# Performance work log

Measured on AMD Instinct MI355X. Metric: run time of the kernel, lower is better.

The kernel has to match this reference:

```python
import jax, jax.numpy as jnp
import numpy as np

NUM_HEADS = 8
GROUPS = 8
EPS = 1e-5


def setup_inputs() -> dict:
    key = jax.random.key(0)
    ks = jax.random.split(key, 5)
    B, C, H, W = 2, 512, 64, 64
    x = jax.random.normal(ks[0], (B, C, H, W), dtype=jnp.float32)
    gn_w = jnp.ones((C,), dtype=jnp.float32)
    gn_b = jnp.zeros((C,), dtype=jnp.float32)
    qkv_w = jax.random.normal(ks[1], (3 * C, C), dtype=jnp.float32) * 0.02  # 1x1 conv weight
    qkv_b = jnp.zeros((3 * C,), dtype=jnp.float32)
    proj_w = jax.random.normal(ks[2], (C, C), dtype=jnp.float32) * 0.02
    proj_b = jnp.zeros((C,), dtype=jnp.float32)
    return {"x": x, "gn_w": gn_w, "gn_b": gn_b, "qkv_w": qkv_w,
            "qkv_b": qkv_b, "proj_w": proj_w, "proj_b": proj_b}


def group_norm(x, w, b):
    B, C, H, W = x.shape
    xg = x.reshape(B, GROUPS, C // GROUPS, H, W)
    mean = xg.mean(axis=(2, 3, 4), keepdims=True)
    var = xg.var(axis=(2, 3, 4), keepdims=True)  # biased, matching torch GroupNorm
    h = ((xg - mean) * jax.lax.rsqrt(var + EPS)).reshape(B, C, H, W)
    return h * w[None, :, None, None] + b[None, :, None, None]


def reference(x, gn_w, gn_b, qkv_w, qkv_b, proj_w, proj_b):
    B, C, H, W = x.shape
    nh = NUM_HEADS
    dh = C // nh
    scale = dh ** -0.5
    S = H * W

    h = group_norm(x, gn_w, gn_b)
    # 1x1 conv == per-pixel linear: (B,3C,H,W)
    qkv = jnp.einsum('bchw,oc->bohw', h, qkv_w) + qkv_b[None, :, None, None]
    qkv = qkv.reshape(B, 3, nh, dh, S)
    q = jnp.swapaxes(qkv[:, 0], -1, -2)  # (B, nh, S, dh)
    k = jnp.swapaxes(qkv[:, 1], -1, -2)
    v = jnp.swapaxes(qkv[:, 2], -1, -2)

    attn = jax.nn.softmax(jnp.einsum('bhsd,btd->bhst', q, k.reshape(B * nh, S, dh).reshape(B, nh, S, dh)) * scale, axis=-1) if False else jax.nn.softmax(jnp.einsum('bhsd,bhtd->bhst', q, k) * scale, axis=-1)
    out = jnp.einsum('bhst,bhtd->bhsd', attn, v)  # (B, nh, S, dh)
    out = jnp.swapaxes(out, -1, -2).reshape(B, C, H, W)
    out = jnp.einsum('bchw,oc->bohw', out, proj_w) + proj_b[None, :, None, None]
    return x + out
```

## Files before the change

### kernel.cpp

```cpp
#include <hip/hip_runtime.h>
#include <hip/hip_bf16.h>

typedef __attribute__((ext_vector_type(4)))  float  f32x4;
typedef __attribute__((ext_vector_type(16))) float  f32x16;
typedef __attribute__((ext_vector_type(8)))  short  s16x8;
typedef __attribute__((ext_vector_type(4)))  short  s16x4;
typedef __attribute__((ext_vector_type(4)))  unsigned u32x4;
typedef __attribute__((ext_vector_type(2)))  unsigned u32x2;

__device__ __forceinline__ float bf2f(short v) {
    unsigned u = ((unsigned)(unsigned short)v) << 16;
    return __builtin_bit_cast(float, u);
}
__device__ __forceinline__ short f2bf(float f) {
    unsigned u = __builtin_bit_cast(unsigned, f);
    u += 0x7fff + ((u >> 16) & 1);
    return (short)(u >> 16);
}
__device__ __forceinline__ unsigned cvt_pk_bf16(float lo, float hi) {
    unsigned r;
    asm("v_cvt_pk_bf16_f32 %0, %1, %2" : "=v"(r) : "v"(lo), "v"(hi));
    return r;
}
__device__ __forceinline__ float exp2_asm(float x) {
    float r; asm("v_exp_f32 %0, %1" : "=v"(r) : "v"(x)); return r;
}
__device__ __forceinline__ float log2_asm(float x) {
    float r; asm("v_log_f32 %0, %1" : "=v"(r) : "v"(x)); return r;
}
__device__ __forceinline__ float max3f(float a, float b, float c) {
    float r; asm("v_max3_f32 %0, %1, %2, %3" : "=v"(r) : "v"(a), "v"(b), "v"(c));
    return r;
}
__device__ __forceinline__ void perm32swap(unsigned &a, unsigned &b) {
    u32x2 r = __builtin_amdgcn_permlane32_swap(a, b, false, false);
    a = r[0]; b = r[1];
}
__device__ __forceinline__ void gload16(const short* g, short* l) {
    __builtin_amdgcn_global_load_lds(
        (const __attribute__((address_space(1))) void*)g,
        (__attribute__((address_space(3))) void*)l, 16, 0, 0);
}

#define BATCH 2
#define CCH   512
#define SSP   4096
#define NH    8
#define DH    64

__global__ __launch_bounds__(256) void wcast_kernel(
    const float* __restrict__ qw, const float* __restrict__ pw,
    short* __restrict__ dq, short* __restrict__ dp)
{
    int idx = (blockIdx.x * 256 + threadIdx.x) * 8;
    const float* src; short* dst;
    if (idx < 786432) { src = qw + idx; dst = dq + idx; }
    else              { src = pw + (idx - 786432); dst = dp + (idx - 786432); }
    f32x4 a = *(const f32x4*)src;
    f32x4 b = *(const f32x4*)(src + 4);
    s16x8 o;
    o[0]=f2bf(a[0]); o[1]=f2bf(a[1]); o[2]=f2bf(a[2]); o[3]=f2bf(a[3]);
    o[4]=f2bf(b[0]); o[5]=f2bf(b[1]); o[6]=f2bf(b[2]); o[7]=f2bf(b[3]);
    *(s16x8*)dst = o;
}

__global__ __launch_bounds__(256) void gn_partial_kernel(
    const float* __restrict__ x, float* __restrict__ part)
{
    int bg = blockIdx.x >> 5, chunk = blockIdx.x & 31;
    const float* base = x + (size_t)bg * 262144 + chunk * 8192;
    int t = threadIdx.x, lane = t & 63, wave = t >> 6;
    float s = 0.f, ss = 0.f;
    #pragma unroll
    for (int k = 0; k < 8; ++k) {
        f32x4 v = *(const f32x4*)&base[k * 1024 + t * 4];
        #pragma unroll
        for (int j = 0; j < 4; ++j) { s += v[j]; ss += v[j] * v[j]; }
    }
    #pragma unroll
    for (int mask = 1; mask < 64; mask <<= 1) {
        s  += __shfl_xor(s,  mask);
        ss += __shfl_xor(ss, mask);
    }
    __shared__ float rs[4], rss[4];
    if (lane == 0) { rs[wave] = s; rss[wave] = ss; }
    __syncthreads();
    if (t == 0) {
        part[blockIdx.x * 2]     = rs[0] + rs[1] + rs[2] + rs[3];
        part[blockIdx.x * 2 + 1] = rss[0] + rss[1] + rss[2] + rss[3];
    }
}

__global__ void gn_final_kernel(const float* __restrict__ part, float* __restrict__ stats)
{
    int t = threadIdx.x;
    if (t < 16) {
        float s = 0.f, ss = 0.f;
        for (int c = 0; c < 32; ++c) {
            s  += part[(t * 32 + c) * 2];
            ss += part[(t * 32 + c) * 2 + 1];
        }
        float mean = s * (1.f / 262144.f);
        float var  = ss * (1.f / 262144.f) - mean * mean;
        stats[t * 2]     = mean;
        stats[t * 2 + 1] = rsqrtf(var + 1e-5f);
    }
}

__global__ __launch_bounds__(256) void gn_apply_kernel(
    const float* __restrict__ x, const float* __restrict__ gw, const float* __restrict__ gb,
    const float* __restrict__ stats, short* __restrict__ hbuf)
{
    __shared__ float tile[64][65];
    int id = blockIdx.x;
    int st = id & 63, ct = (id >> 6) & 7, b = id >> 9;
    int t  = threadIdx.x;
    float mean = stats[(b * 8 + ct) * 2], rstd = stats[(b * 8 + ct) * 2 + 1];
    #pragma unroll
    for (int pass = 0; pass < 4; ++pass) {
        int cr = pass * 16 + (t >> 4);
        int c  = ct * 64 + cr;
        f32x4 v = *(const f32x4*)&x[((size_t)(b * CCH + c)) * SSP + st * 64 + (t & 15) * 4];
        float w  = gw[c] * rstd;
        float bb = gb[c] - mean * w;
        #pragma unroll
        for (int j = 0; j < 4; ++j) tile[cr][(t & 15) * 4 + j] = v[j] * w + bb;
    }
    __syncthreads();
    int sr = t >> 2, cc0 = (t & 3) * 16;
    s16x8 o0, o1;
    #pragma unroll
    for (int j = 0; j < 8; ++j) {
        o0[j] = f2bf(tile[cc0 + j][sr]);
        o1[j] = f2bf(tile[cc0 + 8 + j][sr]);
    }
    short* dst = &hbuf[(size_t)(b * SSP + st * 64 + sr) * CCH + ct * 64 + cc0];
    *(s16x8*)dst = o0;
    *(s16x8*)(dst + 8) = o1;
}

template<int EPI>
__global__ __launch_bounds__(256) void gemm_bt_kernel(
    const short* __restrict__ A, const short* __restrict__ Bt,
    const float* __restrict__ bias,
    short* __restrict__ qout, short* __restrict__ kout, short* __restrict__ vout,
    const float* __restrict__ xres, float* __restrict__ out,
    int K)
{
    __shared__ short As[2][4096], Bs[2][4096];
    const int t = threadIdx.x;
    const int lane = t & 63, wave = t >> 6;
    const int wm = wave >> 1, wn = wave & 1;
    const int m0 = blockIdx.x * 128, n0 = blockIdx.y * 128;
    const int l15 = lane & 15, lq = lane >> 4;

    const int s0r = ((t >> 6) << 4) | (t & 15),          s0c = (t >> 4) & 3;
    const int s1r = (((256 + t) >> 6) << 4) | (t & 15),  s1c = (t >> 4) & 3;
    const short* ga0 = A  + (size_t)(m0 + s0r) * K + s0c * 8;
    const short* ga1 = A  + (size_t)(m0 + s1r) * K + s1c * 8;
    const short* gb0 = Bt + (size_t)(n0 + s0r) * K + s0c * 8;
    const short* gb1 = Bt + (size_t)(n0 + s1r) * K + s1c * 8;
    const int wofs0 = wave * 512;
    const int wofs1 = 2048 + wave * 512;

    f32x4 acc[4][4];
    #pragma unroll
    for (int i = 0; i < 4; ++i)
        #pragma unroll
        for (int j = 0; j < 4; ++j) acc[i][j] = (f32x4){0.f, 0.f, 0.f, 0.f};

    gload16(ga0, &As[0][wofs0]);
    gload16(ga1, &As[0][wofs1]);
    gload16(gb0, &Bs[0][wofs0]);
    gload16(gb1, &Bs[0][wofs1]);
    asm volatile("s_waitcnt vmcnt(0)" ::: "memory");
    __syncthreads();

    int cur = 0;
    for (int kk = 0; kk < K; kk += 32) {
        int nxt = cur ^ 1;
        if (kk + 32 < K) {
            gload16(ga0 + kk + 32, &As[nxt][wofs0]);
            gload16(ga1 + kk + 32, &As[nxt][wofs1]);
            gload16(gb0 + kk + 32, &Bs[nxt][wofs0]);
            gload16(gb1 + kk + 32, &Bs[nxt][wofs1]);
        }
        s16x8 af[4], bfr[4];
        #pragma unroll
        for (int mt = 0; mt < 4; ++mt) af[mt]  = *(const s16x8*)&As[cur][((wm * 4 + mt) << 9) + lane * 8];
        #pragma unroll
        for (int nt = 0; nt < 4; ++nt) bfr[nt] = *(const s16x8*)&Bs[cur][((wn * 4 + nt) << 9) + lane * 8];
        #pragma unroll
        for (int mt = 0; mt < 4; ++mt)
            #pragma unroll
            for (int nt = 0; nt < 4; ++nt)
                acc[mt][nt] = __builtin_amdgcn_mfma_f32_16x16x32_bf16(af[mt], bfr[nt], acc[mt][nt], 0, 0, 0);
        asm volatile("s_waitcnt vmcnt(0)" ::: "memory");
        __syncthreads();
        cur = nxt;
    }

    #pragma unroll
    for (int mt = 0; mt < 4; ++mt) {
        const int r0 = m0 + wm * 64 + mt * 16 + lq * 4;
        #pragma unroll
        for (int nt = 0; nt < 4; ++nt) {
            const int c = n0 + wn * 64 + nt * 16 + l15;
            float bv = bias[c];
            if (EPI == 0) {
                int bb = r0 >> 12, tloc = r0 & 4095;
                if (c < 512) {
                    #pragma unroll
                    for (int i = 0; i < 4; ++i)
                        qout[(size_t)(r0 + i) * 512 + c] = f2bf(acc[mt][nt][i] + bv);
                } else if (c < 1024) {
                    int hh = (c - 512) >> 6, d = (c - 512) & 63;
                    int T = tloc >> 6, tb = (tloc >> 5) & 1;
                    size_t base = (((size_t)(bb * 8 + hh) * 64 + T) * 8 + tb * 4 + (d >> 4)) * 512
                                  + 256 * ((d >> 3) & 1) + (d & 7);
                    #pragma unroll
                    for (int i = 0; i < 4; ++i)
                        kout[base + ((tloc & 31) + i) * 8] = f2bf(acc[mt][nt][i] + bv);
                } else {
                    int hh = (c - 1024) >> 6, d = (c - 1024) & 63;
                    int T = tloc >> 6, s = (tloc >> 4) & 3, thi = (tloc >> 3) & 1, j0 = tloc & 7;
                    size_t base = (((size_t)(bb * 8 + hh) * 64 + T) * 8 + (d >> 5) * 4 + s) * 512
                                  + ((d & 31) + 32 * thi) * 8 + j0;
                    s16x4 pv;
                    #pragma unroll
                    for (int i = 0; i < 4; ++i) pv[i] = f2bf(acc[mt][nt][i] + bv);
                    *(s16x4*)&vout[base] = pv;
                }
            } else {
                int bb = r0 >> 12, s = r0 & 4095;
                size_t xi = (size_t)(bb * CCH + c) * SSP + s;
                f32x4 xv = *(const f32x4*)&xres[xi];
                f32x4 o  = xv + acc[mt][nt] + bv;
                *(f32x4*)&out[xi] = o;
            }
        }
    }
}

__global__ __launch_bounds__(256, 4) void attn_kernel(
    const short* __restrict__ qbuf, const short* __restrict__ kfrag,
    const short* __restrict__ vfrag,
    short* __restrict__ p0, short* __restrict__ p1, float* __restrict__ aout)
{
    __shared__ short Ks[2][4096];
    __shared__ short Vs[2][4096];
    const int t = threadIdx.x, lane = t & 63, wave = t >> 6;
    const int yy = blockIdx.y, bh = yy & 15, half = yy >> 4;
    const int b = bh >> 3, h = bh & 7;
    const int q0w = blockIdx.x * 128 + wave * 32;
    const int l31 = lane & 31, lh = lane >> 5;
    const int kv0 = half * 2048;

    s16x8 qf[4];
    {
        const short* qp = qbuf + (size_t)(b * SSP + q0w + l31) * 512 + h * 64 + 8 * lh;
        #pragma unroll
        for (int s = 0; s < 4; ++s) {
            s16x8 raw = *(const s16x8*)(qp + 16 * s);
            #pragma unroll
            for (int j = 0; j < 8; ++j) qf[s][j] = f2bf(bf2f(raw[j]) * 0.18033688011112042f);
        }
    }

    const short* kbase = kfrag + (size_t)bh * 262144 + lane * 8;
    const short* vbase = vfrag + (size_t)bh * 262144 + lane * 8;

    f32x16 oacc[2];
    oacc[0] = (f32x16){}; oacc[1] = (f32x16){};
    f32x16 lacc = (f32x16){};
    float nm = 0.f;

    s16x8 ones;
    #pragma unroll
    for (int j = 0; j < 8; ++j) ones[j] = (short)0x3F80;

    {
        const short* kg = kbase + (size_t)(kv0 >> 6) * 4096 + wave * 1024;
        gload16(kg,       &Ks[0][wave * 1024]);
        gload16(kg + 512, &Ks[0][wave * 1024 + 512]);
        const short* vg = vbase + (size_t)(kv0 >> 6) * 4096 + wave * 1024;
        gload16(vg,       &Vs[0][wave * 1024]);
        gload16(vg + 512, &Vs[0][wave * 1024 + 512]);
    }
    asm volatile("s_waitcnt vmcnt(0)" ::: "memory");
    __syncthreads();

    int cur = 0;
    for (int t0 = kv0; t0 < kv0 + 2048; t0 += 64) {
        if (t0 + 64 < kv0 + 2048) {
            int nb = cur ^ 1;
            const short* kg = kbase + (size_t)((t0 + 64) >> 6) * 4096 + wave * 1024;
            gload16(kg,       &Ks[nb][wave * 1024]);
            gload16(kg + 512, &Ks[nb][wave * 1024 + 512]);
            const short* vg = vbase + (size_t)((t0 + 64) >> 6) * 4096 + wave * 1024;
            gload16(vg,       &Vs[nb][wave * 1024]);
            gload16(vg + 512, &Vs[nb][wave * 1024 + 512]);
        }

        f32x16 sacc0, sacc1;
        #pragma unroll
        for (int r = 0; r < 16; ++r) { sacc0[r] = nm; sacc1[r] = nm; }
        __builtin_amdgcn_s_setprio(1);
        #pragma unroll
        for (int s = 0; s < 4; ++s) {
            s16x8 k0 = *(const s16x8*)&Ks[cur][(0 + s) * 512 + lane * 8];
            s16x8 k1 = *(const s16x8*)&Ks[cur][(4 + s) * 512 + lane * 8];
            sacc0 = __builtin_amdgcn_mfma_f32_32x32x16_bf16(k0, qf[s], sacc0, 0, 0, 0);
            sacc1 = __builtin_amdgcn_mfma_f32_32x32x16_bf16(k1, qf[s], sacc1, 0, 0, 0);
        }
        __builtin_amdgcn_s_setprio(0);

        float u0 = max3f(sacc0[0],  sacc0[1],  sacc0[2]);
        float u1 = max3f(sacc0[3],  sacc0[4],  sacc0[5]);
        float u2 = max3f(sacc0[6],  sacc0[7],  sacc0[8]);
        float u3 = max3f(sacc0[9],  sacc0[10], sacc0[11]);
        float u4 = max3f(sacc0[12], sacc0[13], sacc0[14]);
        float u5 = max3f(sacc1[0],  sacc1[1],  sacc1[2]);
        float u6 = max3f(sacc1[3],  sacc1[4],  sacc1[5]);
        float u7 = max3f(sacc1[6],  sacc1[7],  sacc1[8]);
        float u8 = max3f(sacc1[9],  sacc1[10], sacc1[11]);
        float u9 = max3f(sacc1[12], sacc1[13], sacc1[14]);
        float ua = fmaxf(sacc0[15], sacc1[15]);
        float v0 = max3f(u0, u1, u2);
        float v1 = max3f(u3, u4, u5);
        float v2 = max3f(u6, u7, u8);
        float v3 = max3f(u9, ua, v0);
        float mx = max3f(v1, v2, v3);

        int calm = __all(mx <= 11.5f);
        if (!calm) {
            float g = fmaxf(mx, __shfl_xor(mx, 32));
            float adj = fmaxf(g, 0.f);
            float corr = exp2_asm(-adj);
            nm -= adj;
            #pragma unroll
            for (int r = 0; r < 16; ++r) { oacc[0][r] *= corr; oacc[1][r] *= corr; }
            lacc[0] *= corr;
            #pragma unroll
            for (int r = 0; r < 16; ++r) { sacc0[r] -= adj; sacc1[r] -= adj; }
        }
        #pragma unroll
        for (int r = 0; r < 16; ++r) { sacc0[r] = exp2_asm(sacc0[r]); sacc1[r] = exp2_asm(sacc1[r]); }

        unsigned w[16];
        #pragma unroll
        for (int r = 0; r < 8; ++r) {
            w[r]     = cvt_pk_bf16(sacc0[2 * r], sacc0[2 * r + 1]);
            w[8 + r] = cvt_pk_bf16(sacc1[2 * r], sacc1[2 * r + 1]);
        }
        #pragma unroll
        for (int s = 0; s < 4; ++s) {
            perm32swap(w[s * 4 + 0], w[s * 4 + 2]);
            perm32swap(w[s * 4 + 1], w[s * 4 + 3]);
        }

        __builtin_amdgcn_s_setprio(1);
        #pragma unroll
        for (int s = 0; s < 4; ++s) {
            u32x4 pb = { w[s * 4 + 0], w[s * 4 + 1], w[s * 4 + 2], w[s * 4 + 3] };
            s16x8 pB = __builtin_bit_cast(s16x8, pb);
            s16x8 v0v = *(const s16x8*)&Vs[cur][(0 + s) * 512 + lane * 8];
            s16x8 v1v = *(const s16x8*)&Vs[cur][(4 + s) * 512 + lane * 8];
            oacc[0] = __builtin_amdgcn_mfma_f32_32x32x16_bf16(v0v, pB, oacc[0], 0, 0, 0);
            oacc[1] = __builtin_amdgcn_mfma_f32_32x32x16_bf16(v1v, pB, oacc[1], 0, 0, 0);
            lacc    = __builtin_amdgcn_mfma_f32_32x32x16_bf16(ones, pB, lacc, 0, 0, 0);
        }
        __builtin_amdgcn_s_setprio(0);

        asm volatile("s_waitcnt vmcnt(0)" ::: "memory");
        __syncthreads();
        cur ^= 1;
    }

    short* pO = half ? p1 : p0;
    float l_ = lacc[0];
    float linv = 1.f / l_;
    int q = q0w + l31;
    size_t obase = ((size_t)bh * 4096 + q) * 64;
    #pragma unroll
    for (int db = 0; db < 2; ++db)
        #pragma unroll
        for (int g = 0; g < 4; ++g) {
            s16x4 o;
            #pragma unroll
            for (int i = 0; i < 4; ++i) o[i] = f2bf(oacc[db][g * 4 + i] * linv);
            *(s16x4*)&pO[obase + db * 32 + g * 8 + lh * 4] = o;
        }
    if (lh == 0)
        aout[half * 65536 + bh * 4096 + q] = -nm + log2_asm(l_);
}

__global__ __launch_bounds__(256) void combine_kernel(
    const short* __restrict__ p0, const short* __restrict__ p1,
    const float* __restrict__ aout, short* __restrict__ ao)
{
    int bh = blockIdx.x >> 7, q = (blockIdx.x & 127) * 32 + (threadIdx.x >> 3);
    int d0 = (threadIdx.x & 7) * 8;
    size_t pi = ((size_t)bh * 4096 + q) * 64 + d0;
    s16x8 o1 = *(const s16x8*)&p0[pi];
    s16x8 o2 = *(const s16x8*)&p1[pi];
    float a1 = aout[bh * 4096 + q], a2 = aout[65536 + bh * 4096 + q];
    float M = fmaxf(a1, a2);
    float w1 = exp2_asm(a1 - M), w2 = exp2_asm(a2 - M);
    float inv = 1.f / (w1 + w2);
    w1 *= inv; w2 *= inv;
    s16x8 o;
    #pragma unroll
    for (int j = 0; j < 8; ++j) o[j] = f2bf(bf2f(o1[j]) * w1 + bf2f(o2[j]) * w2);
    int b = bh >> 3, h = bh & 7;
    *(s16x8*)&ao[(size_t)(b * SSP + q) * 512 + h * 64 + d0] = o;
}

extern "C" void kernel_launch(void* const* d_in, const int* in_sizes, int n_in,
                              void* d_out, int out_size, void* d_ws, size_t ws_size,
                              hipStream_t stream)
{
    (void)in_sizes; (void)n_in; (void)out_size; (void)ws_size;
    const float* x      = (const float*)d_in[0];
    const float* gn_w   = (const float*)d_in[1];
    const float* gn_b   = (const float*)d_in[2];
    const float* qkv_w  = (const float*)d_in[3];
    const float* qkv_b  = (const float*)d_in[4];
    const float* proj_w = (const float*)d_in[5];
    const float* proj_b = (const float*)d_in[6];
    float* out = (float*)d_out;
    char* ws = (char*)d_ws;

    short* hbuf  = (short*)(ws + 0);
    short* qbuf  = (short*)(ws + 8388608);
    short* kfrag = (short*)(ws + 16777216);
    short* vfrag = (short*)(ws + 25165824);
    short* aobuf = (short*)(ws + 33554432);
    short* wqkv  = (short*)(ws + 41943040);
    short* wproj = (short*)(ws + 43515904);
    float* part  = (float*)(ws + 44040192);
    float* stats = (float*)(ws + 44044288);
    float* ascal = (float*)(ws + 41943040);

    wcast_kernel<<<512, 256, 0, stream>>>(qkv_w, proj_w, wqkv, wproj);
    gn_partial_kernel<<<512, 256, 0, stream>>>(x, part);
    gn_final_kernel<<<1, 64, 0, stream>>>(part, stats);
    gn_apply_kernel<<<1024, 256, 0, stream>>>(x, gn_w, gn_b, stats, hbuf);
    gemm_bt_kernel<0><<<dim3(64, 12), 256, 0, stream>>>(hbuf, wqkv, qkv_b,
                                                        qbuf, kfrag, vfrag, nullptr, nullptr, 512);
    attn_kernel<<<dim3(32, 32), 256, 0, stream>>>(qbuf, kfrag, vfrag,
                                                  hbuf, aobuf, ascal);
    combine_kernel<<<2048, 256, 0, stream>>>(hbuf, aobuf, ascal, kfrag);
    gemm_bt_kernel<1><<<dim3(64, 4), 256, 0, stream>>>(kfrag, wproj, proj_b,
                                                       nullptr, nullptr, nullptr, x, out, 512);
}
```

Before: 162.4 us.

## Replace double-buffered direct-to-LDS GEMM loads with single-buffer register staging

The GEMM kernel drops its double-buffered shared-memory pipeline, which used direct global-to-LDS loads (gload16) to prefetch the next K-slice during compute. It now uses one buffer, loading each K-slice through registers into LDS between two barriers per iteration. This halves LDS use and may allow more blocks per CU, but global load latency is no longer overlapped with the MFMA work inside a block.

```diff
diff --git a/kernel.cpp b/kernel.cpp
--- a/kernel.cpp
+++ b/kernel.cpp
@@ -147,57 +147,40 @@
     const float* __restrict__ xres, float* __restrict__ out,
     int K)
 {
-    __shared__ short As[2][4096], Bs[2][4096];
+    __shared__ short As[4096], Bs[4096];
     const int t = threadIdx.x;
     const int lane = t & 63, wave = t >> 6;
     const int wm = wave >> 1, wn = wave & 1;
     const int m0 = blockIdx.x * 128, n0 = blockIdx.y * 128;
     const int l15 = lane & 15, lq = lane >> 4;
 
-    const int s0r = ((t >> 6) << 4) | (t & 15),          s0c = (t >> 4) & 3;
-    const int s1r = (((256 + t) >> 6) << 4) | (t & 15),  s1c = (t >> 4) & 3;
-    const short* ga0 = A  + (size_t)(m0 + s0r) * K + s0c * 8;
-    const short* ga1 = A  + (size_t)(m0 + s1r) * K + s1c * 8;
-    const short* gb0 = Bt + (size_t)(n0 + s0r) * K + s0c * 8;
-    const short* gb1 = Bt + (size_t)(n0 + s1r) * K + s1c * 8;
-    const int wofs0 = wave * 512;
-    const int wofs1 = 2048 + wave * 512;
-
     f32x4 acc[4][4];
     #pragma unroll
     for (int i = 0; i < 4; ++i)
         #pragma unroll
         for (int j = 0; j < 4; ++j) acc[i][j] = (f32x4){0.f, 0.f, 0.f, 0.f};
 
-    gload16(ga0, &As[0][wofs0]);
-    gload16(ga1, &As[0][wofs1]);
-    gload16(gb0, &Bs[0][wofs0]);
-    gload16(gb1, &Bs[0][wofs1]);
-    asm volatile("s_waitcnt vmcnt(0)" ::: "memory");
-    __syncthreads();
-
-    int cur = 0;
     for (int kk = 0; kk < K; kk += 32) {
-        int nxt = cur ^ 1;
-        if (kk + 32 < K) {
-            gload16(ga0 + kk + 32, &As[nxt][wofs0]);
-            gload16(ga1 + kk + 32, &As[nxt][wofs1]);
-            gload16(gb0 + kk + 32, &Bs[nxt][wofs0]);
-            gload16(gb1 + kk + 32, &Bs[nxt][wofs1]);
-        }
+        __syncthreads();
+        #pragma unroll
+        for (int i = 0; i < 2; ++i) {
+            int idx = i * 256 + t;
+            int row = idx >> 2, cb = idx & 3;
+            int dst = ((row >> 4) << 9) + ((((row & 15)) | (cb << 4)) << 3);
+            *(s16x8*)&As[dst] = *(const s16x8*)&A [(size_t)(m0 + row) * K + kk + cb * 8];
+            *(s16x8*)&Bs[dst] = *(const s16x8*)&Bt[(size_t)(n0 + row) * K + kk + cb * 8];
+        }
+        __syncthreads();
         s16x8 af[4], bfr[4];
         #pragma unroll
-        for (int mt = 0; mt < 4; ++mt) af[mt]  = *(const s16x8*)&As[cur][((wm * 4 + mt) << 9) + lane * 8];
-        #pragma unroll
-        for (int nt = 0; nt < 4; ++nt) bfr[nt] = *(const s16x8*)&Bs[cur][((wn * 4 + nt) << 9) + lane * 8];
+        for (int mt = 0; mt < 4; ++mt) af[mt]  = *(const s16x8*)&As[(((wm * 4 + mt) << 9) + lane * 8)];
+        #pragma unroll
+        for (int nt = 0; nt < 4; ++nt) bfr[nt] = *(const s16x8*)&Bs[(((wn * 4 + nt) << 9) + lane * 8)];
         #pragma unroll
         for (int mt = 0; mt < 4; ++mt)
             #pragma unroll
             for (int nt = 0; nt < 4; ++nt)
                 acc[mt][nt] = __builtin_amdgcn_mfma_f32_16x16x32_bf16(af[mt], bfr[nt], acc[mt][nt], 0, 0, 0);
-        asm volatile("s_waitcnt vmcnt(0)" ::: "memory");
-        __syncthreads();
-        cur = nxt;
     }
 
     #pragma unroll
```

After: 158.0 us. 2.7% less time.
